# Kernel optimization log

Measured on AMD Instinct MI355X. Metric: run time of the kernel, lower is better.

## Reference

```python
import jax, jax.numpy as jnp
import numpy as np

B, N, C, K, WDIM = 8, 2048, 128, 16, 512
FOUT = 128  # Fin == Fout required by the residual connection
SQRT2 = float(np.sqrt(2.0))


def lrelu(v):
    # StyleGAN-style 'lrelu' activation: slope 0.2, gain sqrt(2)
    return jax.nn.leaky_relu(v, 0.2) * SQRT2


def layernorm(v, eps=1e-5):
    mu = jnp.mean(v, axis=-1, keepdims=True)
    var = jnp.var(v, axis=-1, keepdims=True)
    return (v - mu) * jax.lax.rsqrt(var + eps)


def setup_inputs() -> dict:
    key = jax.random.key(0)
    ks = jax.random.split(key, 16)
    def lin(k, fan_in, fan_out):
        # fold StyleGAN runtime 1/sqrt(fan_in) weight scaling into init
        return jax.random.normal(k, (fan_in, fan_out), jnp.float32) / np.sqrt(fan_in)
    return {
        "x": jax.random.normal(ks[0], (B, N, C), jnp.float32),
        "w": jax.random.normal(ks[1], (B, WDIM), jnp.float32),
        # AdaptiveNorm modulation (gamma residual-init around 1, beta around 0)
        "Wg": lin(ks[2], WDIM, C),
        "Wb": lin(ks[3], WDIM, C),
        # conv_w: Fin -> Fout//2 (lrelu) -> Fout (linear), 1x1 convs == per-edge linear
        "W1": lin(ks[4], C, FOUT // 2), "b1": jnp.zeros((FOUT // 2,), jnp.float32),
        "W2": lin(ks[5], FOUT // 2, FOUT), "b2": jnp.zeros((FOUT,), jnp.float32),
        # conv_x: 2*Fin -> Fout (lrelu) -> Fout (linear)
        "Wx1": lin(ks[6], 2 * C, FOUT), "bx1": jnp.zeros((FOUT,), jnp.float32),
        "Wx2": lin(ks[7], FOUT, FOUT), "bx2": jnp.zeros((FOUT,), jnp.float32),
        # layer-scale FC(512 -> Fout); original weight_init=0, randomized here
        # so gradients/outputs are non-trivial for kernel testing
        "Wls": lin(ks[8], WDIM, FOUT), "bls": jnp.zeros((FOUT,), jnp.float32),
    }


def reference(x, w, Wg, Wb, W1, b1, W2, b2, Wx1, bx1, Wx2, bx2, Wls, bls):
    # AdaptiveNorm: layernorm modulated by style w
    h = layernorm(x) * (1.0 + w @ Wg)[:, None, :] + (w @ Wb)[:, None, :]  # [B,N,C]

    # ---- get_edge_features: pairwise sq-dist -> kNN (excluding self) ----
    sq = jnp.sum(h * h, axis=-1)                                   # [B,N]
    dist = sq[:, :, None] - 2.0 * jnp.einsum('bnc,bmc->bnm', h, h) + sq[:, None, :]
    _, idx = jax.lax.top_k(-dist, K + 1)                           # [B,N,K+1]
    idx = idx[..., 1:]                                             # drop self -> [B,N,K]

    nbr = jax.vmap(lambda hb, ib: hb[ib])(h, idx)                  # [B,N,K,C]
    central = h[:, :, None, :]                                     # [B,N,1,C]
    delta = nbr - central                                          # [B,N,K,C]

    # ---- conv_w on the delta half, softmax over neighbors ----
    hw = lrelu(delta @ W1 + b1)
    wlog = hw @ W2 + b2                                            # [B,N,K,FOUT]
    wsm = jax.nn.softmax(wlog.astype(jnp.float32), axis=2).astype(x.dtype)

    # ---- conv_x on [central, delta] edge features ----
    ee = jnp.concatenate([jnp.broadcast_to(central, delta.shape), delta], axis=-1)
    hx = lrelu(ee @ Wx1 + bx1)
    xe = hx @ Wx2 + bx2                                            # [B,N,K,FOUT]

    agg = jnp.sum(xe * wsm, axis=2)                                # [B,N,FOUT]
    return agg * (w @ Wls + bls)[:, None, :] + x
```

## Files before the change

### kernel.cpp

```cpp
#include <hip/hip_runtime.h>

#define Bz 8
#define Nn 2048
#define Cc 128
#define KK 16
#define WD 512
#define F2 64
#define FO 128
#define NP (Bz*Nn)
#define SQ2 1.41421356237309515f
#define HSTRIDE 136
#define CAPMAX 256

#define GOFF   ((size_t)0)
#define BEOFF  ((size_t)1024)
#define LSOFF  ((size_t)2048)
#define HOFF   ((size_t)3072)
#define SQOFF  (HOFF + (size_t)NP*Cc)
#define A1OFF  (SQOFF + (size_t)NP)
#define ADOFF  (A1OFF + (size_t)NP*F2)
#define HXOFF  (ADOFF + (size_t)NP*Cc)
#define IXOFF  (HXOFF + (size_t)NP*Cc)
#define CNTOFF (IXOFF + (size_t)NP*KK)
#define FBNOFF (CNTOFF + (size_t)NP)
#define FBQOFF (FBNOFF + (size_t)64)
#define HIBYTES   ((FBQOFF + (size_t)NP) * 4)
#define W2TBYTES  (HIBYTES + (size_t)NP*HSTRIDE*2)
#define WX2TBYTES (W2TBYTES + (size_t)128*64*2)
#define CANDBYTES (WX2TBYTES + (size_t)128*128*2)

typedef __attribute__((ext_vector_type(8))) short bf16x8;
typedef __attribute__((ext_vector_type(4))) float f32x4;

__device__ __forceinline__ unsigned short f2bf(float f) {
  unsigned u = __float_as_uint(f);
  unsigned r = (u + 0x7FFFu + ((u >> 16) & 1u)) >> 16;
  return (unsigned short)r;
}
__device__ __forceinline__ float lrelu(float v) {
  return (v > 0.f ? v : 0.2f*v) * SQ2;
}

__global__ __launch_bounds__(512) void k_pervec(const float* __restrict__ w,
    const float* __restrict__ Wg, const float* __restrict__ Wb,
    const float* __restrict__ Wls, const float* __restrict__ bls,
    float* __restrict__ ws) {
  __shared__ float red[3][4][Cc];
  const int b = blockIdx.x;
  const int c = threadIdx.x & 127, dc = threadIdx.x >> 7;
  const float* wr = w + b*WD;
  float ag = 0.f, ab = 0.f, al = 0.f;
  for (int d = dc*128; d < dc*128 + 128; ++d) {
    float wv = wr[d];
    ag = fmaf(wv, Wg[d*Cc + c], ag);
    ab = fmaf(wv, Wb[d*Cc + c], ab);
    al = fmaf(wv, Wls[d*Cc + c], al);
  }
  red[0][dc][c] = ag; red[1][dc][c] = ab; red[2][dc][c] = al;
  __syncthreads();
  if (dc == 0) {
    float sg = red[0][0][c] + red[0][1][c] + red[0][2][c] + red[0][3][c];
    float sb = red[1][0][c] + red[1][1][c] + red[1][2][c] + red[1][3][c];
    float sl = red[2][0][c] + red[2][1][c] + red[2][2][c] + red[2][3][c];
    ws[GOFF  + b*Cc + c] = 1.0f + sg;
    ws[BEOFF + b*Cc + c] = sb;
    ws[LSOFF + b*Cc + c] = sl + bls[c];
  }
}

__global__ __launch_bounds__(256) void k_wprep(const float* __restrict__ W2,
    const float* __restrict__ Wx2, unsigned short* __restrict__ w2t,
    unsigned short* __restrict__ wx2t) {
  int idx = blockIdx.x*256 + threadIdx.x;
  if (idx < 128*64)  { int c = idx >> 6, j = idx & 63;  w2t[idx]  = f2bf(W2[j*FO + c]); }
  if (idx < 128*128) { int c = idx >> 7, j = idx & 127; wx2t[idx] = f2bf(Wx2[j*FO + c]); }
}

__global__ __launch_bounds__(64) void k_h(const float* __restrict__ x,
                                          float* __restrict__ ws,
                                          unsigned short* __restrict__ hi_g,
                                          int* __restrict__ fbn) {
  const int n = blockIdx.x;
  const int b = n >> 11;
  const int t = threadIdx.x;
  if (n == 0 && t == 0) fbn[0] = 0;
  const float* xr = x + (size_t)n*Cc;
  float x0 = xr[t], x1 = xr[t + 64];
  float s = x0 + x1, ss = x0*x0 + x1*x1;
  #pragma unroll
  for (int m = 1; m < 64; m <<= 1) {
    s  += __shfl_xor(s,  m, 64);
    ss += __shfl_xor(ss, m, 64);
  }
  float mu  = s * (1.0f/128.0f);
  float var = ss * (1.0f/128.0f) - mu*mu;
  float rs  = rsqrtf(var + 1e-5f);
  float h0 = (x0 - mu)*rs*ws[GOFF + b*Cc + t]      + ws[BEOFF + b*Cc + t];
  float h1 = (x1 - mu)*rs*ws[GOFF + b*Cc + t + 64] + ws[BEOFF + b*Cc + t + 64];
  float* hr = ws + HOFF + (size_t)n*Cc;
  hr[t] = h0; hr[t + 64] = h1;
  hi_g[(size_t)n*HSTRIDE + t]      = f2bf(h0);
  hi_g[(size_t)n*HSTRIDE + t + 64] = f2bf(h1);
  float q = h0*h0 + h1*h1;
  #pragma unroll
  for (int m = 1; m < 64; m <<= 1) q += __shfl_xor(q, m, 64);
  if (t == 0) ws[SQOFF + n] = q;
}

__global__ __launch_bounds__(128) void k_pre(const float* __restrict__ W1,
    const float* __restrict__ Wx1, const float* __restrict__ bx1,
    float* __restrict__ ws) {
  __shared__ float hs[4][Cc];
  const int t = threadIdx.x;
  const size_t row0 = (size_t)blockIdx.x * 4;
  const float* h = ws + HOFF;
  #pragma unroll
  for (int r = 0; r < 4; ++r) hs[r][t] = h[(row0 + r)*Cc + t];
  __syncthreads();
  float ad[4] = {0,0,0,0}, ac[4] = {0,0,0,0};
  for (int cp = 0; cp < Cc; ++cp) {
    float whi = Wx1[cp*FO + t];
    float wlo = Wx1[(Cc + cp)*FO + t];
    #pragma unroll
    for (int r = 0; r < 4; ++r) {
      float hv = hs[r][cp];
      ac[r] = fmaf(hv, whi, ac[r]);
      ad[r] = fmaf(hv, wlo, ad[r]);
    }
  }
  float bx = bx1[t];
  #pragma unroll
  for (int r = 0; r < 4; ++r) {
    ws[ADOFF + (row0 + r)*Cc + t] = ad[r];
    ws[HXOFF + (row0 + r)*Cc + t] = ac[r] - ad[r] + bx;
  }
  const int j = t & 63, rp = t >> 6;
  float a0 = 0.f, a1 = 0.f;
  for (int cp = 0; cp < Cc; ++cp) {
    float wv = W1[cp*F2 + j];
    a0 = fmaf(hs[rp][cp],     wv, a0);
    a1 = fmaf(hs[rp + 2][cp], wv, a1);
  }
  ws[A1OFF + (row0 + rp)*F2 + j]     = a0;
  ws[A1OFF + (row0 + rp + 2)*F2 + j] = a1;
}

__global__ __launch_bounds__(512, 4) void k_filter(float* __restrict__ ws,
    const unsigned short* __restrict__ hi_g, unsigned short* __restrict__ cand,
    int* __restrict__ cnt_g, int CAP) {
  __shared__ unsigned short hiA[32*HSTRIDE];
  __shared__ float smB[8704];
  __shared__ float sqA[32], sqB[128], tauS[32];
  __shared__ int cnt[32];
  unsigned short* hB = (unsigned short*)smB;
  float* dstage = smB;
  const int t = threadIdx.x;
  const int b  = blockIdx.x >> 6;
  const int i0 = (blockIdx.x & 63) << 5;
  const int wave = t >> 6, lane = t & 63;
  const int wi = wave & 1, wj = wave >> 1;
  const int l15 = lane & 15, l4 = lane >> 4;
  const float* __restrict__ sq = ws + SQOFF + (size_t)b*Nn;
  const unsigned short* __restrict__ hib = hi_g + (size_t)b*Nn*HSTRIDE;

  {
    int r = t >> 4, o = (t & 15) * 8;
    *(bf16x8*)&hiA[r*HSTRIDE + o] = *(const bf16x8*)&hib[(size_t)(i0 + r)*HSTRIDE + o];
  }
  if (t < 32) { sqA[t] = sq[i0 + t]; cnt[t] = 0; }

  float samp[4][8];

  for (int jt = 0; jt < 4; ++jt) {
    const int j0 = jt << 7;
    __syncthreads();
    { int r = t >> 2, o = (t & 3) * 32;
      #pragma unroll
      for (int q = 0; q < 4; ++q)
        *(bf16x8*)&hB[r*HSTRIDE + o + q*8] =
            *(const bf16x8*)&hib[(size_t)(j0 + r)*HSTRIDE + o + q*8];
    }
    if (t < 128) sqB[t] = sq[j0 + t];
    __syncthreads();
    f32x4 acc0 = {0,0,0,0}, acc1 = {0,0,0,0};
    #pragma unroll
    for (int kb = 0; kb < 4; ++kb) {
      const int cbase = kb*32 + l4*8;
      bf16x8 a  = *(const bf16x8*)&hiA[(16*wi + l15)*HSTRIDE + cbase];
      bf16x8 b0 = *(const bf16x8*)&hB [(32*wj      + l15)*HSTRIDE + cbase];
      bf16x8 b1 = *(const bf16x8*)&hB [(32*wj + 16 + l15)*HSTRIDE + cbase];
      acc0 = __builtin_amdgcn_mfma_f32_16x16x32_bf16(a, b0, acc0, 0, 0, 0);
      acc1 = __builtin_amdgcn_mfma_f32_16x16x32_bf16(a, b1, acc1, 0, 0, 0);
    }
    __syncthreads();
    #pragma unroll
    for (int jb = 0; jb < 2; ++jb) {
      const f32x4 a = jb ? acc1 : acc0;
      #pragma unroll
      for (int r = 0; r < 4; ++r) {
        int il = 16*wi + l4*4 + r;
        int jl = 32*wj + 16*jb + l15;
        dstage[il*132 + jl] = sqA[il] + sqB[jl] - 2.f*a[r];
      }
    }
    __syncthreads();
    #pragma unroll
    for (int r = 0; r < 4; ++r) {
      int row = wave*4 + r;
      samp[r][jt*2]     = dstage[row*132 + lane];
      samp[r][jt*2 + 1] = dstage[row*132 + 64 + lane];
    }
  }

  {
    float lo[4], hi[4];
    #pragma unroll
    for (int r = 0; r < 4; ++r) {
      float m = samp[r][0];
      #pragma unroll
      for (int k = 1; k < 8; ++k) m = fmaxf(m, samp[r][k]);
      #pragma unroll
      for (int s2 = 1; s2 < 64; s2 <<= 1) m = fmaxf(m, __shfl_xor(m, s2, 64));
      hi[r] = fmaxf(m, 0.f)*1.0001f + 1e-6f;
      lo[r] = 0.f;
    }
    #pragma unroll 1
    for (int it = 0; it < 18; ++it) {
      float mid[4], cv[4];
      #pragma unroll
      for (int r = 0; r < 4; ++r) {
        mid[r] = 0.5f*(lo[r] + hi[r]);
        float c = 0.f;
        #pragma unroll
        for (int k = 0; k < 8; ++k) c += (samp[r][k] < mid[r]) ? 1.f : 0.f;
        cv[r] = c;
      }
      #pragma unroll
      for (int s2 = 1; s2 < 64; s2 <<= 1) {
        #pragma unroll
        for (int r = 0; r < 4; ++r) cv[r] += __shfl_xor(cv[r], s2, 64);
      }
      #pragma unroll
      for (int r = 0; r < 4; ++r) {
        bool ge = cv[r] >= 20.f;
        hi[r] = ge ? mid[r] : hi[r];
        lo[r] = ge ? lo[r] : mid[r];
      }
    }
    if (lane == 0) {
      #pragma unroll
      for (int r = 0; r < 4; ++r) tauS[wave*4 + r] = hi[r];
    }
    __syncthreads();
    #pragma unroll
    for (int r = 0; r < 4; ++r) {
      int row = wave*4 + r;
      float tv = hi[r];
      size_t rg = (size_t)(b*Nn + i0 + row);
      #pragma unroll
      for (int k = 0; k < 8; ++k) {
        if (samp[r][k] < tv) {
          int j = (k >> 1)*128 + (k & 1)*64 + lane;
          int pos = atomicAdd(&cnt[row], 1);
          if (pos < CAP) cand[rg*CAPMAX + pos] = (unsigned short)j;
        }
      }
    }
  }

  for (int jt = 4; jt < 16; ++jt) {
    const int j0 = jt << 7;
    __syncthreads();
    { int r = t >> 2, o = (t & 3) * 32;
      #pragma unroll
      for (int q = 0; q < 4; ++q)
        *(bf16x8*)&hB[r*HSTRIDE + o + q*8] =
            *(const bf16x8*)&hib[(size_t)(j0 + r)*HSTRIDE + o + q*8];
    }
    if (t < 128) sqB[t] = sq[j0 + t];
    __syncthreads();
    f32x4 acc0 = {0,0,0,0}, acc1 = {0,0,0,0};
    #pragma unroll
    for (int kb = 0; kb < 4; ++kb) {
      const int cbase = kb*32 + l4*8;
      bf16x8 a  = *(const bf16x8*)&hiA[(16*wi + l15)*HSTRIDE + cbase];
      bf16x8 b0 = *(const bf16x8*)&hB [(32*wj      + l15)*HSTRIDE + cbase];
      bf16x8 b1 = *(const bf16x8*)&hB [(32*wj + 16 + l15)*HSTRIDE + cbase];
      acc0 = __builtin_amdgcn_mfma_f32_16x16x32_bf16(a, b0, acc0, 0, 0, 0);
      acc1 = __builtin_amdgcn_mfma_f32_16x16x32_bf16(a, b1, acc1, 0, 0, 0);
    }
    #pragma unroll
    for (int jb = 0; jb < 2; ++jb) {
      const f32x4 a = jb ? acc1 : acc0;
      #pragma unroll
      for (int r = 0; r < 4; ++r) {
        int il = 16*wi + l4*4 + r;
        int jl = 32*wj + 16*jb + l15;
        float dv = sqA[il] + sqB[jl] - 2.f*a[r];
        if (dv < tauS[il]) {
          int pos = atomicAdd(&cnt[il], 1);
          if (pos < CAP)
            cand[(size_t)(b*Nn + i0 + il)*CAPMAX + pos] = (unsigned short)(j0 + jl);
        }
      }
    }
  }
  __syncthreads();
  if (t < 32) cnt_g[b*Nn + i0 + t] = cnt[t];
}

__global__ __launch_bounds__(256) void k_refine(float* __restrict__ ws,
    const unsigned short* __restrict__ cand, const int* __restrict__ cnt_g,
    int* __restrict__ fbn, int* __restrict__ fbq, int CAP) {
  __shared__ float dsh[4][CAPMAX];
  __shared__ unsigned short cjs[4][CAPMAX];
  const int wave = threadIdx.x >> 6, lane = threadIdx.x & 63;
  const int s8 = lane >> 3, ch = lane & 7;
  const int blk = blockIdx.x;
  const int row = ((blk & 7)*512 + (blk >> 3))*4 + wave;
  const int b = row >> 11;
  const float* __restrict__ h = ws + HOFF;
  int c_ = cnt_g[row];
  int cm = (c_ < 17 || c_ > CAP) ? 0 : c_;
  if (cm == 0 && lane == 0) { int q = atomicAdd(fbn, 1); fbq[q] = row; }
  for (int cc = lane; cc < cm; cc += 64)
    cjs[wave][cc] = cand[(size_t)row*CAPMAX + cc];
  float4 hi4[4];
  #pragma unroll
  for (int q = 0; q < 4; ++q)
    hi4[q] = *(const float4*)&h[(size_t)row*Cc + ch*4 + q*32];
  __syncthreads();
  const int np8 = (cm + 7) >> 3;
  for (int p = 0; p < np8; ++p) {
    int slot = p*8 + s8;
    int sl = slot < cm ? slot : 0;
    int jj = cjs[wave][sl];
    const float* hj = h + (size_t)(b*Nn + jj)*Cc;
    float part = 0.f;
    #pragma unroll
    for (int q = 0; q < 4; ++q) {
      float4 v = *(const float4*)&hj[ch*4 + q*32];
      float e0 = hi4[q].x - v.x, e1 = hi4[q].y - v.y;
      float e2 = hi4[q].z - v.z, e3 = hi4[q].w - v.w;
      part = fmaf(e0, e0, part); part = fmaf(e1, e1, part);
      part = fmaf(e2, e2, part); part = fmaf(e3, e3, part);
    }
    part += __shfl_xor(part, 1, 64);
    part += __shfl_xor(part, 2, 64);
    part += __shfl_xor(part, 4, 64);
    if (ch == 0 && slot < cm) dsh[wave][slot] = part;
  }
  __syncthreads();
  int* op = (int*)(ws + IXOFF) + (size_t)row*KK;
  for (int cc = lane; cc < cm; cc += 64) {
    float dc = dsh[wave][cc];
    int jc = cjs[wave][cc];
    int rank = 0;
    #pragma unroll 1
    for (int m = 0; m < cm; ++m) {
      float dm = dsh[wave][m];
      int jm = cjs[wave][m];
      rank += (dm < dc || (dm == dc && jm < jc)) ? 1 : 0;
    }
    if (rank >= 1 && rank <= 16) op[rank - 1] = b*Nn + jc;
  }
}

__global__ __launch_bounds__(256) void k_fb(float* __restrict__ ws,
    const int* __restrict__ fbn, const int* __restrict__ fbq) {
  __shared__ float fd[4][17];
  __shared__ int   fj[4][17];
  __shared__ float his[128];
  const int wave = threadIdx.x >> 6, lane = threadIdx.x & 63;
  int nfb = fbn[0];
  nfb = (nfb < 0) ? 0 : ((nfb > NP) ? NP : nfb);
  for (int q = blockIdx.x; q < nfb; q += gridDim.x) {
    const int row = fbq[q];
    if ((unsigned)row >= (unsigned)NP) continue;
    const int b = row >> 11;
    const float* __restrict__ h = ws + HOFF + (size_t)b*Nn*Cc;
    if (threadIdx.x < 128) his[threadIdx.x] = h[(size_t)(row & (Nn-1))*Cc + threadIdx.x];
    __syncthreads();
    const float hi0 = his[lane], hi1 = his[lane + 64];
    float td[17]; int tj[17];
    #pragma unroll
    for (int s = 0; s < 17; ++s) { td[s] = 3.0e38f; tj[s] = 0x7FFFFFFF; }
    float cmax = 3.0e38f; int cjm = 0x7FFFFFFF, cpos = 0;
    const int jb = wave*512;
    #pragma unroll 1
    for (int it = 0; it < 256; ++it) {
      int j = jb + it*2;
      float a0 = h[(size_t)j*Cc + lane],     a1 = h[(size_t)j*Cc + lane + 64];
      float b0 = h[(size_t)(j+1)*Cc + lane], b1 = h[(size_t)(j+1)*Cc + lane + 64];
      float e0 = hi0 - a0, e1 = hi1 - a1, f0 = hi0 - b0, f1 = hi1 - b1;
      float p0 = e0*e0; p0 = fmaf(e1, e1, p0);
      float p1 = f0*f0; p1 = fmaf(f1, f1, p1);
      #pragma unroll
      for (int s2 = 1; s2 < 64; s2 <<= 1) {
        p0 += __shfl_xor(p0, s2, 64);
        p1 += __shfl_xor(p1, s2, 64);
      }
      #pragma unroll
      for (int u = 0; u < 2; ++u) {
        float d = u ? p1 : p0;
        int jd = j + u;
        if (d < cmax || (d == cmax && jd < cjm)) {
          #pragma unroll
          for (int s = 0; s < 17; ++s) {
            bool r = (s == cpos);
            td[s] = r ? d  : td[s];
            tj[s] = r ? jd : tj[s];
          }
          cmax = td[0]; cjm = tj[0]; cpos = 0;
          #pragma unroll
          for (int s = 1; s < 17; ++s)
            if (td[s] > cmax || (td[s] == cmax && tj[s] > cjm)) {
              cmax = td[s]; cjm = tj[s]; cpos = s;
            }
        }
      }
    }
    if (lane == 0) {
      #pragma unroll
      for (int s = 0; s < 17; ++s) { fd[wave][s] = td[s]; fj[wave][s] = tj[s]; }
    }
    __syncthreads();
    if (threadIdx.x < 68) {
      int e = threadIdx.x;
      float dc = fd[e / 17][e % 17];
      int   jc = fj[e / 17][e % 17];
      int rank = 0;
      #pragma unroll 1
      for (int m = 0; m < 68; ++m) {
        float dm = fd[m / 17][m % 17];
        int jm = fj[m / 17][m % 17];
        rank += (dm < dc || (dm == dc && jm < jc)) ? 1 : 0;
      }
      if (rank >= 1 && rank <= 16) {
        int* op = (int*)(ws + IXOFF) + (size_t)row*KK;
        op[rank - 1] = b*Nn + jc;
      }
    }
    __syncthreads();
  }
}

__global__ __launch_bounds__(256) void k_mlp(
    const float* __restrict__ b1v, const float* __restrict__ bx2,
    const unsigned short* __restrict__ w2t, const unsigned short* __restrict__ wx2t,
    const float* __restrict__ x, float* __restrict__ out,
    float* __restrict__ ws) {
  const int wave = threadIdx.x >> 6, lane = threadIdx.x & 63;
  const int blk = blockIdx.x;
  const int n = ((blk & 7)*512 + (blk >> 3))*4 + wave;
  const int b = n >> 11;
  const int l15 = lane & 15, l4 = lane >> 4;
  const int* __restrict__ ip = (const int*)(ws + IXOFF) + (size_t)n*KK;
  const int mk = ip[l15];

  const float* __restrict__ A1 = ws + A1OFF;
  const float* a1m = A1 + (size_t)mk*F2;
  const float* a1n = A1 + (size_t)n*F2;
  bf16x8 hwA[2];
  #pragma unroll
  for (int c = 0; c < 2; ++c) {
    int off = c*32 + l4*8;
    float4 p0 = *(const float4*)(a1m + off), p1 = *(const float4*)(a1m + off + 4);
    float4 q0 = *(const float4*)(a1n + off), q1 = *(const float4*)(a1n + off + 4);
    float4 b0 = *(const float4*)(b1v + off), b1_ = *(const float4*)(b1v + off + 4);
    bf16x8 r;
    r[0] = (short)f2bf(lrelu(p0.x - q0.x + b0.x));
    r[1] = (short)f2bf(lrelu(p0.y - q0.y + b0.y));
    r[2] = (short)f2bf(lrelu(p0.z - q0.z + b0.z));
    r[3] = (short)f2bf(lrelu(p0.w - q0.w + b0.w));
    r[4] = (short)f2bf(lrelu(p1.x - q1.x + b1_.x));
    r[5] = (short)f2bf(lrelu(p1.y - q1.y + b1_.y));
    r[6] = (short)f2bf(lrelu(p1.z - q1.z + b1_.z));
    r[7] = (short)f2bf(lrelu(p1.w - q1.w + b1_.w));
    hwA[c] = r;
  }
  const float* adm = ws + ADOFF + (size_t)mk*Cc;
  const float* hxb = ws + HXOFF + (size_t)n*Cc;
  bf16x8 hxA[4];
  #pragma unroll
  for (int c = 0; c < 4; ++c) {
    int off = c*32 + l4*8;
    float4 p0 = *(const float4*)(adm + off), p1 = *(const float4*)(adm + off + 4);
    float4 q0 = *(const float4*)(hxb + off), q1 = *(const float4*)(hxb + off + 4);
    bf16x8 r;
    r[0] = (short)f2bf(lrelu(p0.x + q0.x));
    r[1] = (short)f2bf(lrelu(p0.y + q0.y));
    r[2] = (short)f2bf(lrelu(p0.z + q0.z));
    r[3] = (short)f2bf(lrelu(p0.w + q0.w));
    r[4] = (short)f2bf(lrelu(p1.x + q1.x));
    r[5] = (short)f2bf(lrelu(p1.y + q1.y));
    r[6] = (short)f2bf(lrelu(p1.z + q1.z));
    r[7] = (short)f2bf(lrelu(p1.w + q1.w));
    hxA[c] = r;
  }

  f32x4 wl[8];
  #pragma unroll
  for (int nt = 0; nt < 8; ++nt) {
    f32x4 acc = {0,0,0,0};
    acc = __builtin_amdgcn_mfma_f32_16x16x32_bf16(hwA[0],
            *(const bf16x8*)&w2t[(size_t)(nt*16 + l15)*64 + l4*8], acc, 0, 0, 0);
    acc = __builtin_amdgcn_mfma_f32_16x16x32_bf16(hwA[1],
            *(const bf16x8*)&w2t[(size_t)(nt*16 + l15)*64 + 32 + l4*8], acc, 0, 0, 0);
    wl[nt] = acc;
  }
  #pragma unroll
  for (int nt = 0; nt < 8; ++nt) {
    float mx = fmaxf(fmaxf(wl[nt][0], wl[nt][1]), fmaxf(wl[nt][2], wl[nt][3]));
    mx = fmaxf(mx, __shfl_xor(mx, 16, 64));
    mx = fmaxf(mx, __shfl_xor(mx, 32, 64));
    float e0 = __expf(wl[nt][0] - mx), e1 = __expf(wl[nt][1] - mx);
    float e2 = __expf(wl[nt][2] - mx), e3 = __expf(wl[nt][3] - mx);
    float sm = e0 + e1 + e2 + e3;
    sm += __shfl_xor(sm, 16, 64);
    sm += __shfl_xor(sm, 32, 64);
    float rs = 1.0f / sm;
    wl[nt][0] = e0*rs; wl[nt][1] = e1*rs; wl[nt][2] = e2*rs; wl[nt][3] = e3*rs;
  }

  #pragma unroll
  for (int nt = 0; nt < 8; ++nt) {
    f32x4 acc = {0,0,0,0};
    #pragma unroll
    for (int c = 0; c < 4; ++c)
      acc = __builtin_amdgcn_mfma_f32_16x16x32_bf16(hxA[c],
              *(const bf16x8*)&wx2t[(size_t)(nt*16 + l15)*128 + c*32 + l4*8],
              acc, 0, 0, 0);
    int col = nt*16 + l15;
    float bx = bx2[col];
    float ap = wl[nt][0]*(acc[0] + bx) + wl[nt][1]*(acc[1] + bx)
             + wl[nt][2]*(acc[2] + bx) + wl[nt][3]*(acc[3] + bx);
    ap += __shfl_xor(ap, 16, 64);
    ap += __shfl_xor(ap, 32, 64);
    if (l4 == 0) {
      size_t xo = (size_t)n*Cc + col;
      out[xo] = fmaf(ap, ws[LSOFF + b*Cc + col], x[xo]);
    }
  }
}

extern "C" void kernel_launch(void* const* d_in, const int* in_sizes, int n_in,
                              void* d_out, int out_size, void* d_ws, size_t ws_size,
                              hipStream_t stream) {
  const float* x   = (const float*)d_in[0];
  const float* w   = (const float*)d_in[1];
  const float* Wg  = (const float*)d_in[2];
  const float* Wb  = (const float*)d_in[3];
  const float* W1  = (const float*)d_in[4];
  const float* b1  = (const float*)d_in[5];
  const float* W2  = (const float*)d_in[6];
  const float* Wx1 = (const float*)d_in[8];
  const float* bx1 = (const float*)d_in[9];
  const float* Wx2 = (const float*)d_in[10];
  const float* bx2 = (const float*)d_in[11];
  const float* Wls = (const float*)d_in[12];
  const float* bls = (const float*)d_in[13];
  float* out = (float*)d_out;
  float* ws  = (float*)d_ws;
  unsigned short* hi_g = (unsigned short*)((char*)d_ws + HIBYTES);
  unsigned short* w2t  = (unsigned short*)((char*)d_ws + W2TBYTES);
  unsigned short* wx2t = (unsigned short*)((char*)d_ws + WX2TBYTES);
  unsigned short* cand = (unsigned short*)((char*)d_ws + CANDBYTES);
  int* cnt_g = (int*)(ws + CNTOFF);
  int* fbn   = (int*)(ws + FBNOFF);
  int* fbq   = (int*)(ws + FBQOFF);

  int CAP = 0;
  if (ws_size > CANDBYTES) {
    size_t c = (ws_size - CANDBYTES) / ((size_t)NP * 2);
    CAP = (c >= CAPMAX) ? CAPMAX : (int)c;
  }

  k_pervec<<<Bz, 512, 0, stream>>>(w, Wg, Wb, Wls, bls, ws);
  k_wprep<<<64, 256, 0, stream>>>(W2, Wx2, w2t, wx2t);
  k_h<<<NP, 64, 0, stream>>>(x, ws, hi_g, fbn);
  k_pre<<<NP/4, 128, 0, stream>>>(W1, Wx1, bx1, ws);
  k_filter<<<512, 512, 0, stream>>>(ws, hi_g, cand, cnt_g, CAP);
  k_refine<<<NP/4, 256, 0, stream>>>(ws, cand, cnt_g, fbn, fbq, CAP);
  k_fb<<<256, 256, 0, stream>>>(ws, fbn, fbq);
  k_mlp<<<NP/4, 256, 0, stream>>>(b1, bx2, w2t, wx2t, x, out, ws);
}
```

Baseline: 438.1 us.

## Stage MLP weights in LDS and loop 8 points per wave in k_mlp

k_mlp now launches 512 blocks instead of NP/4, and each wave processes 8 consecutive points. Each block first copies the W2 and Wx2 bf16 weights into padded shared memory, and the MFMA B-operand reads come from LDS instead of global memory. Biases and layer-scale values are hoisted out of the loop, and the next neighbor index is prefetched. This amortizes weight loads across points, at the cost of fewer blocks, about 53KB of LDS per block (limiting occupancy), and a serial per-wave loop.

```diff
diff --git a/kernel.cpp b/kernel.cpp
--- a/kernel.cpp
+++ b/kernel.cpp
@@ -163,8 +163,7 @@
   const float* __restrict__ sq = ws + SQOFF + (size_t)b*Nn;
   const unsigned short* __restrict__ hib = hi_g + (size_t)b*Nn*HSTRIDE;
 
-  {
-    int r = t >> 4, o = (t & 15) * 8;
+  { int r = t >> 4, o = (t & 15) * 8;
     *(bf16x8*)&hiA[r*HSTRIDE + o] = *(const bf16x8*)&hib[(size_t)(i0 + r)*HSTRIDE + o];
   }
   if (t < 32) { sqA[t] = sq[i0 + t]; cnt[t] = 0; }
@@ -445,102 +444,136 @@
   }
 }
 
+#define W2S_STRIDE  72
+#define WX2S_STRIDE 136
 __global__ __launch_bounds__(256) void k_mlp(
     const float* __restrict__ b1v, const float* __restrict__ bx2,
     const unsigned short* __restrict__ w2t, const unsigned short* __restrict__ wx2t,
     const float* __restrict__ x, float* __restrict__ out,
     float* __restrict__ ws) {
+  __shared__ unsigned short w2s[128*W2S_STRIDE];
+  __shared__ unsigned short wx2s[128*WX2S_STRIDE];
   const int wave = threadIdx.x >> 6, lane = threadIdx.x & 63;
+  const int l15 = lane & 15, l4 = lane >> 4;
   const int blk = blockIdx.x;
-  const int n = ((blk & 7)*512 + (blk >> 3))*4 + wave;
-  const int b = n >> 11;
-  const int l15 = lane & 15, l4 = lane >> 4;
-  const int* __restrict__ ip = (const int*)(ws + IXOFF) + (size_t)n*KK;
-  const int mk = ip[l15];
-
-  const float* __restrict__ A1 = ws + A1OFF;
-  const float* a1m = A1 + (size_t)mk*F2;
-  const float* a1n = A1 + (size_t)n*F2;
-  bf16x8 hwA[2];
+  const int bb = blk & 7;
+  const int nbase = bb*Nn + (blk >> 3)*32 + wave*8;
+
+  for (int i = threadIdx.x*8; i < 128*64; i += 256*8) {
+    int j = i >> 6, k = i & 63;
+    *(bf16x8*)&w2s[j*W2S_STRIDE + k] = *(const bf16x8*)&w2t[i];
+  }
+  for (int i = threadIdx.x*8; i < 128*128; i += 256*8) {
+    int j = i >> 7, k = i & 127;
+    *(bf16x8*)&wx2s[j*WX2S_STRIDE + k] = *(const bf16x8*)&wx2t[i];
+  }
+
+  float4 b1f[4];
   #pragma unroll
   for (int c = 0; c < 2; ++c) {
-    int off = c*32 + l4*8;
-    float4 p0 = *(const float4*)(a1m + off), p1 = *(const float4*)(a1m + off + 4);
-    float4 q0 = *(const float4*)(a1n + off), q1 = *(const float4*)(a1n + off + 4);
-    float4 b0 = *(const float4*)(b1v + off), b1_ = *(const float4*)(b1v + off + 4);
-    bf16x8 r;
-    r[0] = (short)f2bf(lrelu(p0.x - q0.x + b0.x));
-    r[1] = (short)f2bf(lrelu(p0.y - q0.y + b0.y));
-    r[2] = (short)f2bf(lrelu(p0.z - q0.z + b0.z));
-    r[3] = (short)f2bf(lrelu(p0.w - q0.w + b0.w));
-    r[4] = (short)f2bf(lrelu(p1.x - q1.x + b1_.x));
-    r[5] = (short)f2bf(lrelu(p1.y - q1.y + b1_.y));
-    r[6] = (short)f2bf(lrelu(p1.z - q1.z + b1_.z));
-    r[7] = (short)f2bf(lrelu(p1.w - q1.w + b1_.w));
-    hwA[c] = r;
-  }
-  const float* adm = ws + ADOFF + (size_t)mk*Cc;
-  const float* hxb = ws + HXOFF + (size_t)n*Cc;
-  bf16x8 hxA[4];
-  #pragma unroll
-  for (int c = 0; c < 4; ++c) {
-    int off = c*32 + l4*8;
-    float4 p0 = *(const float4*)(adm + off), p1 = *(const float4*)(adm + off + 4);
-    float4 q0 = *(const float4*)(hxb + off), q1 = *(const float4*)(hxb + off + 4);
-    bf16x8 r;
-    r[0] = (short)f2bf(lrelu(p0.x + q0.x));
-    r[1] = (short)f2bf(lrelu(p0.y + q0.y));
-    r[2] = (short)f2bf(lrelu(p0.z + q0.z));
-    r[3] = (short)f2bf(lrelu(p0.w + q0.w));
-    r[4] = (short)f2bf(lrelu(p1.x + q1.x));
-    r[5] = (short)f2bf(lrelu(p1.y + q1.y));
-    r[6] = (short)f2bf(lrelu(p1.z + q1.z));
-    r[7] = (short)f2bf(lrelu(p1.w + q1.w));
-    hxA[c] = r;
-  }
-
-  f32x4 wl[8];
+    b1f[c*2]     = *(const float4*)(b1v + c*32 + l4*8);
+    b1f[c*2 + 1] = *(const float4*)(b1v + c*32 + l4*8 + 4);
+  }
+  float bxv[8], lsv[8];
   #pragma unroll
   for (int nt = 0; nt < 8; ++nt) {
-    f32x4 acc = {0,0,0,0};
-    acc = __builtin_amdgcn_mfma_f32_16x16x32_bf16(hwA[0],
-            *(const bf16x8*)&w2t[(size_t)(nt*16 + l15)*64 + l4*8], acc, 0, 0, 0);
-    acc = __builtin_amdgcn_mfma_f32_16x16x32_bf16(hwA[1],
-            *(const bf16x8*)&w2t[(size_t)(nt*16 + l15)*64 + 32 + l4*8], acc, 0, 0, 0);
-    wl[nt] = acc;
-  }
-  #pragma unroll
-  for (int nt = 0; nt < 8; ++nt) {
-    float mx = fmaxf(fmaxf(wl[nt][0], wl[nt][1]), fmaxf(wl[nt][2], wl[nt][3]));
-    mx = fmaxf(mx, __shfl_xor(mx, 16, 64));
-    mx = fmaxf(mx, __shfl_xor(mx, 32, 64));
-    float e0 = __expf(wl[nt][0] - mx), e1 = __expf(wl[nt][1] - mx);
-    float e2 = __expf(wl[nt][2] - mx), e3 = __expf(wl[nt][3] - mx);
-    float sm = e0 + e1 + e2 + e3;
-    sm += __shfl_xor(sm, 16, 64);
-    sm += __shfl_xor(sm, 32, 64);
-    float rs = 1.0f / sm;
-    wl[nt][0] = e0*rs; wl[nt][1] = e1*rs; wl[nt][2] = e2*rs; wl[nt][3] = e3*rs;
-  }
-
-  #pragma unroll
-  for (int nt = 0; nt < 8; ++nt) {
-    f32x4 acc = {0,0,0,0};
-    #pragma unroll
-    for (int c = 0; c < 4; ++c)
-      acc = __builtin_amdgcn_mfma_f32_16x16x32_bf16(hxA[c],
-              *(const bf16x8*)&wx2t[(size_t)(nt*16 + l15)*128 + c*32 + l4*8],
-              acc, 0, 0, 0);
-    int col = nt*16 + l15;
-    float bx = bx2[col];
-    float ap = wl[nt][0]*(acc[0] + bx) + wl[nt][1]*(acc[1] + bx)
-             + wl[nt][2]*(acc[2] + bx) + wl[nt][3]*(acc[3] + bx);
-    ap += __shfl_xor(ap, 16, 64);
-    ap += __shfl_xor(ap, 32, 64);
-    if (l4 == 0) {
-      size_t xo = (size_t)n*Cc + col;
-      out[xo] = fmaf(ap, ws[LSOFF + b*Cc + col], x[xo]);
-    }
+    bxv[nt] = bx2[nt*16 + l15];
+    lsv[nt] = ws[LSOFF + bb*Cc + nt*16 + l15];
+  }
+  __syncthreads();
+
+  const int* __restrict__ ipg = (const int*)(ws + IXOFF);
+  const float* __restrict__ A1 = ws + A1OFF;
+  int mk = ipg[(size_t)nbase*KK + l15];
+
+  #pragma unroll 1
+  for (int p = 0; p < 8; ++p) {
+    const int n = nbase + p;
+    int mk_next = (p < 7) ? ipg[(size_t)(n + 1)*KK + l15] : 0;
+
+    const float* a1m = A1 + (size_t)mk*F2;
+    const float* a1n = A1 + (size_t)n*F2;
+    bf16x8 hwA[2];
+    #pragma unroll
+    for (int c = 0; c < 2; ++c) {
+      int off = c*32 + l4*8;
+      float4 p0 = *(const float4*)(a1m + off), p1 = *(const float4*)(a1m + off + 4);
+      float4 q0 = *(const float4*)(a1n + off), q1 = *(const float4*)(a1n + off + 4);
+      float4 b0 = b1f[c*2], b1_ = b1f[c*2 + 1];
+      bf16x8 r;
+      r[0] = (short)f2bf(lrelu(p0.x - q0.x + b0.x));
+      r[1] = (short)f2bf(lrelu(p0.y - q0.y + b0.y));
+      r[2] = (short)f2bf(lrelu(p0.z - q0.z + b0.z));
+      r[3] = (short)f2bf(lrelu(p0.w - q0.w + b0.w));
+      r[4] = (short)f2bf(lrelu(p1.x - q1.x + b1_.x));
+      r[5] = (short)f2bf(lrelu(p1.y - q1.y + b1_.y));
+      r[6] = (short)f2bf(lrelu(p1.z - q1.z + b1_.z));
+      r[7] = (short)f2bf(lrelu(p1.w - q1.w + b1_.w));
+      hwA[c] = r;
+    }
+    const float* adm = ws + ADOFF + (size_t)mk*Cc;
+    const float* hxb = ws + HXOFF + (size_t)n*Cc;
+    bf16x8 hxA[4];
+    #pragma unroll
+    for (int c = 0; c < 4; ++c) {
+      int off = c*32 + l4*8;
+      float4 p0 = *(const float4*)(adm + off), p1 = *(const float4*)(adm + off + 4);
+      float4 q0 = *(const float4*)(hxb + off), q1 = *(const float4*)(hxb + off + 4);
+      bf16x8 r;
+      r[0] = (short)f2bf(lrelu(p0.x + q0.x));
+      r[1] = (short)f2bf(lrelu(p0.y + q0.y));
+      r[2] = (short)f2bf(lrelu(p0.z + q0.z));
+      r[3] = (short)f2bf(lrelu(p0.w + q0.w));
+      r[4] = (short)f2bf(lrelu(p1.x + q1.x));
+      r[5] = (short)f2bf(lrelu(p1.y + q1.y));
+      r[6] = (short)f2bf(lrelu(p1.z + q1.z));
+      r[7] = (short)f2bf(lrelu(p1.w + q1.w));
+      hxA[c] = r;
+    }
+
+    f32x4 wl[8];
+    #pragma unroll
+    for (int nt = 0; nt < 8; ++nt) {
+      f32x4 acc = {0,0,0,0};
+      acc = __builtin_amdgcn_mfma_f32_16x16x32_bf16(hwA[0],
+              *(const bf16x8*)&w2s[(nt*16 + l15)*W2S_STRIDE + l4*8], acc, 0, 0, 0);
+      acc = __builtin_amdgcn_mfma_f32_16x16x32_bf16(hwA[1],
+              *(const bf16x8*)&w2s[(nt*16 + l15)*W2S_STRIDE + 32 + l4*8], acc, 0, 0, 0);
+      wl[nt] = acc;
+    }
+    #pragma unroll
+    for (int nt = 0; nt < 8; ++nt) {
+      float mx = fmaxf(fmaxf(wl[nt][0], wl[nt][1]), fmaxf(wl[nt][2], wl[nt][3]));
+      mx = fmaxf(mx, __shfl_xor(mx, 16, 64));
+      mx = fmaxf(mx, __shfl_xor(mx, 32, 64));
+      float e0 = __expf(wl[nt][0] - mx), e1 = __expf(wl[nt][1] - mx);
+      float e2 = __expf(wl[nt][2] - mx), e3 = __expf(wl[nt][3] - mx);
+      float sm = e0 + e1 + e2 + e3;
+      sm += __shfl_xor(sm, 16, 64);
+      sm += __shfl_xor(sm, 32, 64);
+      float rs = 1.0f / sm;
+      wl[nt][0] = e0*rs; wl[nt][1] = e1*rs; wl[nt][2] = e2*rs; wl[nt][3] = e3*rs;
+    }
+
+    #pragma unroll
+    for (int nt = 0; nt < 8; ++nt) {
+      f32x4 acc = {0,0,0,0};
+      #pragma unroll
+      for (int c = 0; c < 4; ++c)
+        acc = __builtin_amdgcn_mfma_f32_16x16x32_bf16(hxA[c],
+                *(const bf16x8*)&wx2s[(nt*16 + l15)*WX2S_STRIDE + c*32 + l4*8],
+                acc, 0, 0, 0);
+      float bx = bxv[nt];
+      float ap = wl[nt][0]*(acc[0] + bx) + wl[nt][1]*(acc[1] + bx)
+               + wl[nt][2]*(acc[2] + bx) + wl[nt][3]*(acc[3] + bx);
+      ap += __shfl_xor(ap, 16, 64);
+      ap += __shfl_xor(ap, 32, 64);
+      if (l4 == 0) {
+        size_t xo = (size_t)n*Cc + nt*16 + l15;
+        out[xo] = fmaf(ap, lsv[nt], x[xo]);
+      }
+    }
+    mk = mk_next;
   }
 }
 
@@ -583,5 +616,5 @@
   k_filter<<<512, 512, 0, stream>>>(ws, hi_g, cand, cnt_g, CAP);
   k_refine<<<NP/4, 256, 0, stream>>>(ws, cand, cnt_g, fbn, fbq, CAP);
   k_fb<<<256, 256, 0, stream>>>(ws, fbn, fbq);
-  k_mlp<<<NP/4, 256, 0, stream>>>(b1, bx2, w2t, wx2t, x, out, ws);
-}
+  k_mlp<<<512, 256, 0, stream>>>(b1, bx2, w2t, wx2t, x, out, ws);
+}
```

After: 419.5 us. 1.04x faster.
